# Kernel tuning notes

Hardware: AMD Instinct MI355X
Metric: run time of the kernel (lower is better)

The kernel has to match this reference:

```python
import jax, jax.numpy as jnp
import numpy as np

B, S, D = 4, 1024, 1024
H = 16
DK = D // H  # per-head dim_q = dim_k = 64
DFF = 4096
EPS = 1e-5


def _layer_norm(x, g, b):
    m = jnp.mean(x, axis=-1, keepdims=True)
    v = jnp.mean((x - m) ** 2, axis=-1, keepdims=True)
    return (x - m) / jnp.sqrt(v + EPS) * g + b


def setup_inputs() -> dict:
    key = jax.random.key(0)
    ks = jax.random.split(key, 16)
    sd = 1.0 / np.sqrt(D)
    sk = 1.0 / np.sqrt(H * DK)
    sf = 1.0 / np.sqrt(DFF)
    return {
        "src": jax.random.normal(ks[0], (B, S, D), jnp.float32),
        # stacked per-head projections (torch loops over H separate nn.Linear)
        "Wq": jax.random.uniform(ks[1], (H, D, DK), jnp.float32, -sd, sd),
        "bq": jax.random.uniform(ks[2], (H, DK), jnp.float32, -sd, sd),
        "Wk": jax.random.uniform(ks[3], (H, D, DK), jnp.float32, -sd, sd),
        "bk": jax.random.uniform(ks[4], (H, DK), jnp.float32, -sd, sd),
        "Wv": jax.random.uniform(ks[5], (H, D, DK), jnp.float32, -sd, sd),
        "bv": jax.random.uniform(ks[6], (H, DK), jnp.float32, -sd, sd),
        "Wo": jax.random.uniform(ks[7], (H * DK, D), jnp.float32, -sk, sk),
        "bo": jax.random.uniform(ks[8], (D,), jnp.float32, -sk, sk),
        "g1": jnp.ones((D,), jnp.float32),
        "be1": jnp.zeros((D,), jnp.float32),
        "W1": jax.random.uniform(ks[9], (D, DFF), jnp.float32, -sd, sd),
        "b1": jax.random.uniform(ks[10], (DFF,), jnp.float32, -sd, sd),
        "W2": jax.random.uniform(ks[11], (DFF, D), jnp.float32, -sf, sf),
        "b2": jax.random.uniform(ks[12], (D,), jnp.float32, -sf, sf),
        "g2": jnp.ones((D,), jnp.float32),
        "be2": jnp.zeros((D,), jnp.float32),
    }


def reference(src, Wq, bq, Wk, bk, Wv, bv, Wo, bo, g1, be1, W1, b1, W2, b2, g2, be2):
    # multi-head attention (all heads batched via einsum instead of python loop)
    q = jnp.einsum("bsd,hdk->bhsk", src, Wq) + bq[None, :, None, :]
    k = jnp.einsum("bsd,hdk->bhsk", src, Wk) + bk[None, :, None, :]
    v = jnp.einsum("bsd,hdk->bhsk", src, Wv) + bv[None, :, None, :]
    scale = jnp.asarray(DK, src.dtype) ** 0.5  # query.size(-1) ** 0.5
    scores = jnp.einsum("bhsk,bhtk->bhst", q, k) / scale
    attn = jax.nn.softmax(scores, axis=-1)
    o = jnp.einsum("bhst,bhtk->bhsk", attn, v)  # [B,H,S,DK]
    o = o.transpose(0, 2, 1, 3).reshape(src.shape[0], src.shape[1], H * DK)
    attn_out = o @ Wo + bo
    x = _layer_norm(src + attn_out, g1, be1)
    ffn = jax.nn.relu(x @ W1 + b1) @ W2 + b2
    return _layer_norm(x + ffn, g2, be2)
```

## Files before the change

kernel.cpp:

```cpp
#include <hip/hip_runtime.h>
#include <hip/hip_bf16.h>

#define DEV __device__ __forceinline__

typedef __attribute__((ext_vector_type(8))) short bf16x8;
typedef __attribute__((ext_vector_type(4))) float f32x4;
typedef __attribute__((ext_vector_type(4))) short short4v;
typedef __attribute__((ext_vector_type(2))) unsigned uint2v;

DEV short f2bf(float f) {
    union { float f; unsigned u; } x; x.f = f;
    unsigned u = x.u;
    unsigned r = (u + 0x7fffu + ((u >> 16) & 1u)) >> 16;
    return (short)r;
}

DEV float bf2f(short s) {
    union { unsigned u; float f; } x;
    x.u = ((unsigned)(unsigned short)s) << 16;
    return x.f;
}

DEV unsigned cvtpk(float a, float b) {
    unsigned r;
    asm("v_cvt_pk_bf16_f32 %0, %1, %2" : "=v"(r) : "v"(a), "v"(b));
    return r;
}

#define GLD16(g, l)                                                         \
    __builtin_amdgcn_global_load_lds(                                       \
        (const __attribute__((address_space(1))) void*)(g),                 \
        (__attribute__((address_space(3))) void*)(l), 16, 0, 0)

#define WAITV(n) asm volatile("s_waitcnt vmcnt(" #n ")" ::: "memory")
#define SBAR()   asm volatile("s_barrier" ::: "memory")
#define LGKMDRAIN() asm volatile("s_waitcnt lgkmcnt(0)" ::: "memory")


__global__ __launch_bounds__(256) void k_cast(const float* __restrict__ in,
                                              short* __restrict__ out, int n4) {
    int i = blockIdx.x * 256 + threadIdx.x;
    if (i >= n4) return;
    float4 v = ((const float4*)in)[i];
    short4v o;
    o[0] = f2bf(v.x); o[1] = f2bf(v.y); o[2] = f2bf(v.z); o[3] = f2bf(v.w);
    ((short4v*)out)[i] = o;
}

__global__ __launch_bounds__(256) void k_tr(const float* __restrict__ in,
                                            short* __restrict__ out,
                                            int R, int C,
                                            long in_hs, long out_hs) {
    in  += (size_t)blockIdx.z * in_hs;
    out += (size_t)blockIdx.z * out_hs;
    __shared__ short tile[64][68];
    const int t = threadIdx.x;
    const int r0 = blockIdx.y * 64, c0 = blockIdx.x * 64;
    const int lr = t >> 4, lc4 = (t & 15) * 4;
#pragma unroll
    for (int it = 0; it < 4; ++it) {
        int r = lr + it * 16;
        float4 v = *(const float4*)(in + (size_t)(r0 + r) * C + c0 + lc4);
        tile[lc4 + 0][r] = f2bf(v.x);
        tile[lc4 + 1][r] = f2bf(v.y);
        tile[lc4 + 2][r] = f2bf(v.z);
        tile[lc4 + 3][r] = f2bf(v.w);
    }
    __syncthreads();
#pragma unroll
    for (int it = 0; it < 4; ++it) {
        int c = lr + it * 16;
        short4v o;
        o[0] = tile[c][lc4 + 0];
        o[1] = tile[c][lc4 + 1];
        o[2] = tile[c][lc4 + 2];
        o[3] = tile[c][lc4 + 3];
        *(short4v*)(out + (size_t)(c0 + c) * R + r0 + lc4) = o;
    }
}

__global__ __launch_bounds__(256) void k_tr3(const float* __restrict__ Wq,
                                             const float* __restrict__ Wk,
                                             const float* __restrict__ Wv,
                                             short* __restrict__ out) {
    const int z = blockIdx.z;
    const float* in = ((z < 16) ? Wq : (z < 32) ? Wk : Wv) +
                      (size_t)(z & 15) * 65536;
    short* o = out + (size_t)z * 65536;
    __shared__ short tile[64][68];
    const int t = threadIdx.x;
    const int r0 = blockIdx.y * 64;
    const int lr = t >> 4, lc4 = (t & 15) * 4;
#pragma unroll
    for (int it = 0; it < 4; ++it) {
        int r = lr + it * 16;
        float4 v = *(const float4*)(in + (size_t)(r0 + r) * 64 + lc4);
        tile[lc4 + 0][r] = f2bf(v.x);
        tile[lc4 + 1][r] = f2bf(v.y);
        tile[lc4 + 2][r] = f2bf(v.z);
        tile[lc4 + 3][r] = f2bf(v.w);
    }
    __syncthreads();
#pragma unroll
    for (int it = 0; it < 4; ++it) {
        int c = lr + it * 16;
        short4v ov;
        ov[0] = tile[c][lc4 + 0];
        ov[1] = tile[c][lc4 + 1];
        ov[2] = tile[c][lc4 + 2];
        ov[3] = tile[c][lc4 + 3];
        *(short4v*)(o + (size_t)c * 1024 + r0 + lc4) = ov;
    }
}

template <int MODE>
__global__ __launch_bounds__(512, 2) void k_gemm8(
    const short* __restrict__ A, const short* __restrict__ BT,
    int K, int NT,
    const float* __restrict__ f0, const float* __restrict__ f1,
    const float* __restrict__ f2,
    void* __restrict__ o0, void* __restrict__ o1, void* __restrict__ o2) {
    __shared__ short lds[2][2][2][128 * 64];
    const int t = threadIdx.x;
    const int w = t >> 6, l = t & 63;
    const int l16 = l & 15, lg = l >> 4;
    const int wm = w >> 2, wn = w & 3;
    const int bn = blockIdx.x, bm = blockIdx.y;
    const int koff = blockIdx.z * NT * 64;
    const short* Ab = A + (size_t)bm * 256 * K + koff;
    const short* Bb = BT + (size_t)bn * 256 * K + koff;
    const int srow = l >> 3;
    const int scol = ((l & 7) ^ srow) * 8;
    const int offk0 = ((0 + lg) ^ (l16 & 7)) * 8;
    const int offk1 = ((4 + lg) ^ (l16 & 7)) * 8;

    f32x4 acc[8][4] = {};

    auto stg = [&](int buf, int op, int h, int kt) {
#pragma unroll
        for (int i = 0; i < 2; ++i) {
            int row = h * 128 + w * 16 + i * 8 + srow;
            GLD16((op ? Bb : Ab) + (size_t)row * K + (size_t)kt * 64 + scol,
                  &lds[buf][op][h][(w * 16 + i * 8) * 64]);
        }
    };

    stg(0, 0, 0, 0); stg(0, 0, 1, 0);
    stg(0, 1, 0, 0); stg(0, 1, 1, 0);
    const int t1p = (NT > 1) ? 1 : 0;
    stg(1, 1, 0, t1p); stg(1, 1, 1, t1p);
    WAITV(4);
    SBAR();

    for (int kt = 0; kt < NT; ++kt) {
        const int cur = kt & 1, nxt = cur ^ 1;
        const int t1 = (kt + 1 < NT) ? kt + 1 : NT - 1;
        const int t2 = (kt + 2 < NT) ? kt + 2 : NT - 1;

        stg(nxt, 0, 0, t1); stg(nxt, 0, 1, t1);

        bf16x8 a0[4][2], a1[4][2], b0[2][2], b1[2][2];
#pragma unroll
        for (int m = 0; m < 4; ++m) {
            a0[m][0] = *(const bf16x8*)&lds[cur][0][wm][(m * 16 + l16) * 64 + offk0];
            a0[m][1] = *(const bf16x8*)&lds[cur][0][wm][(m * 16 + l16) * 64 + offk1];
        }
#pragma unroll
        for (int n = 0; n < 2; ++n) {
            int r = (wn & 1) * 64 + n * 16 + l16;
            b0[n][0] = *(const bf16x8*)&lds[cur][1][wn >> 1][r * 64 + offk0];
            b0[n][1] = *(const bf16x8*)&lds[cur][1][wn >> 1][r * 64 + offk1];
            int r2 = (wn & 1) * 64 + (n + 2) * 16 + l16;
            b1[n][0] = *(const bf16x8*)&lds[cur][1][wn >> 1][r2 * 64 + offk0];
            b1[n][1] = *(const bf16x8*)&lds[cur][1][wn >> 1][r2 * 64 + offk1];
        }
        __builtin_amdgcn_s_setprio(1);
#pragma unroll
        for (int m = 0; m < 4; ++m)
#pragma unroll
            for (int n = 0; n < 2; ++n) {
                acc[m][n] = __builtin_amdgcn_mfma_f32_16x16x32_bf16(a0[m][0], b0[n][0], acc[m][n], 0, 0, 0);
                acc[m][n] = __builtin_amdgcn_mfma_f32_16x16x32_bf16(a0[m][1], b0[n][1], acc[m][n], 0, 0, 0);
                acc[m][n + 2] = __builtin_amdgcn_mfma_f32_16x16x32_bf16(a0[m][0], b1[n][0], acc[m][n + 2], 0, 0, 0);
                acc[m][n + 2] = __builtin_amdgcn_mfma_f32_16x16x32_bf16(a0[m][1], b1[n][1], acc[m][n + 2], 0, 0, 0);
            }
        __builtin_amdgcn_s_setprio(0);
#pragma unroll
        for (int m = 0; m < 4; ++m) {
            a1[m][0] = *(const bf16x8*)&lds[cur][0][wm][((m + 4) * 16 + l16) * 64 + offk0];
            a1[m][1] = *(const bf16x8*)&lds[cur][0][wm][((m + 4) * 16 + l16) * 64 + offk1];
        }
        __builtin_amdgcn_s_setprio(1);
#pragma unroll
        for (int m = 0; m < 4; ++m)
#pragma unroll
            for (int n = 0; n < 2; ++n) {
                acc[m + 4][n + 2] = __builtin_amdgcn_mfma_f32_16x16x32_bf16(a1[m][0], b1[n][0], acc[m + 4][n + 2], 0, 0, 0);
                acc[m + 4][n + 2] = __builtin_amdgcn_mfma_f32_16x16x32_bf16(a1[m][1], b1[n][1], acc[m + 4][n + 2], 0, 0, 0);
                acc[m + 4][n] = __builtin_amdgcn_mfma_f32_16x16x32_bf16(a1[m][0], b0[n][0], acc[m + 4][n], 0, 0, 0);
                acc[m + 4][n] = __builtin_amdgcn_mfma_f32_16x16x32_bf16(a1[m][1], b0[n][1], acc[m + 4][n], 0, 0, 0);
            }
        __builtin_amdgcn_s_setprio(0);

        LGKMDRAIN();
        SBAR();
        stg(cur, 1, 0, t2); stg(cur, 1, 1, t2);
        WAITV(4);
        SBAR();
    }
    WAITV(0);

    const int N = gridDim.x * 256;
#pragma unroll
    for (int m = 0; m < 8; ++m) {
        int rowbase = bm * 256 + wm * 128 + m * 16 + lg * 4;
#pragma unroll
        for (int n = 0; n < 4; ++n) {
            int col = bn * 256 + wn * 64 + n * 16 + l16;
            if constexpr (MODE == 0) {
                int p = col >> 10, c1 = col & 1023;
                int hh = c1 >> 6, dk = c1 & 63;
                const float* bias = (p == 0) ? f0 : (p == 1) ? f1 : f2;
                float bvl = bias[c1];
                float qs = (p == 0) ? 0.18033688011112042f : 1.0f;
                int b = rowbase >> 10, s = rowbase & 1023;
                if (p == 2) {
                    short4v vv;
#pragma unroll
                    for (int rr = 0; rr < 4; ++rr) vv[rr] = f2bf(acc[m][n][rr] + bvl);
                    *(short4v*)((short*)o2 + (((size_t)(b * 16 + hh) * 64 + dk) << 10) + s) = vv;
                } else {
                    short* dst = (p == 0) ? (short*)o0 : (short*)o1;
#pragma unroll
                    for (int rr = 0; rr < 4; ++rr)
                        dst[(((size_t)(b * 16 + hh) << 10) + s + rr) * 64 + dk] =
                            f2bf((acc[m][n][rr] + bvl) * qs);
                }
            } else if constexpr (MODE == 2) {
                float bvl = f0[col];
#pragma unroll
                for (int rr = 0; rr < 4; ++rr) {
                    size_t idx = (size_t)(rowbase + rr) * N + col;
                    float y = acc[m][n][rr] + bvl;
                    ((short*)o0)[idx] = f2bf(y > 0.f ? y : 0.f);
                }
            } else {
                const int Mtot = gridDim.y * 256;
                short* dst = (blockIdx.z < 3)
                    ? (short*)o0 + (size_t)blockIdx.z * Mtot * N
                    : (short*)o1;
                size_t base = (size_t)rowbase * N + col;
#pragma unroll
                for (int rr = 0; rr < 4; ++rr)
                    dst[base + (size_t)rr * N] = f2bf(acc[m][n][rr]);
            }
        }
    }
}

__global__ __launch_bounds__(512, 4) void k_attn(const short* __restrict__ Q,
                                                 const short* __restrict__ Kt,
                                                 const short* __restrict__ VT,
                                                 short* __restrict__ O) {
    __shared__ short Kl[2][64 * 64];
    __shared__ short Vl[2][64 * 64];
    __shared__ short Pl[8][16 * 64];
    const int bh = blockIdx.x;
    const int qb = blockIdx.y;
    const int t = threadIdx.x;
    const int w = t >> 6, l = t & 63;
    const int l16 = l & 15, lg = l >> 4;
    const int sw = l16 & 7;
    const int pmask = (l16 & 7) << 1;
    const int srow = l >> 3;
    const int scol = ((l & 7) ^ srow) * 8;

    const short* Qb = Q + ((size_t)bh * 1024 + qb * 128 + w * 16 + l16) * 64 + lg * 8;
    bf16x8 qf0 = *(const bf16x8*)Qb;
    bf16x8 qf1 = *(const bf16x8*)(Qb + 32);

    const short* Kbase = Kt + (size_t)bh * (1024 * 64);
    const short* Vbase = VT + (size_t)bh * (64 * 1024);

    const float THR = 11.5415603f;

    bf16x8 ones;
#pragma unroll
    for (int i = 0; i < 8; ++i) ones[i] = (short)0x3F80;

    float m = -1e30f;
    f32x4 oacc[4] = {};
    f32x4 oaccS = {};

    auto stage = [&](int buf, int t0) {
        int roww = w * 8;
        GLD16(Kbase + (size_t)(t0 + roww + srow) * 64 + scol,
              &Kl[buf][roww * 64]);
        GLD16(Vbase + (size_t)(roww + srow) * 1024 + t0 + scol,
              &Vl[buf][roww * 64]);
    };

    auto compute = [&](int cur) {
        f32x4 s[4];
#pragma unroll
        for (int n = 0; n < 4; ++n) {
            bf16x8 kf0 = *(const bf16x8*)&Kl[cur][(n * 16 + l16) * 64 + (lg ^ sw) * 8];
            bf16x8 kf1 = *(const bf16x8*)&Kl[cur][(n * 16 + l16) * 64 + ((4 + lg) ^ sw) * 8];
            f32x4 a = {0.f, 0.f, 0.f, 0.f};
            a = __builtin_amdgcn_mfma_f32_16x16x32_bf16(kf0, qf0, a, 0, 0, 0);
            a = __builtin_amdgcn_mfma_f32_16x16x32_bf16(kf1, qf1, a, 0, 0, 0);
            s[n] = a;
        }
        float m1 = fmaxf(fmaxf(s[0][0], s[0][1]), s[0][2]);
        float m2 = fmaxf(fmaxf(s[0][3], s[1][0]), s[1][1]);
        float m3 = fmaxf(fmaxf(s[1][2], s[1][3]), s[2][0]);
        float m4 = fmaxf(fmaxf(s[2][1], s[2][2]), s[2][3]);
        float m5 = fmaxf(fmaxf(s[3][0], s[3][1]), s[3][2]);
        float mx = fmaxf(fmaxf(m1, m2), m3);
        mx = fmaxf(fmaxf(m4, m5), fmaxf(mx, s[3][3]));
        mx = fmaxf(mx, __shfl_xor(mx, 16));
        mx = fmaxf(mx, __shfl_xor(mx, 32));

        if (__any(mx > m + THR)) {
            float mn = fmaxf(m, mx);
            float al = exp2f(m - mn);
            m = mn;
#pragma unroll
            for (int n = 0; n < 4; ++n)
#pragma unroll
                for (int r = 0; r < 4; ++r) s[n][r] = exp2f(s[n][r] - m);
#pragma unroll
            for (int r = 0; r < 4; ++r) {
                float alr = __shfl(al, lg * 4 + r);
                oaccS[r] *= alr;
#pragma unroll
                for (int n = 0; n < 4; ++n) oacc[n][r] *= alr;
            }
        } else {
#pragma unroll
            for (int n = 0; n < 4; ++n)
#pragma unroll
                for (int r = 0; r < 4; ++r) s[n][r] = exp2f(s[n][r] - m);
        }
#pragma unroll
        for (int n = 0; n < 4; ++n) {
            uint2v pv;
            pv[0] = cvtpk(s[n][0], s[n][1]);
            pv[1] = cvtpk(s[n][2], s[n][3]);
            int g = (n * 4 + lg) ^ pmask;
            *(uint2v*)((char*)Pl[w] + l16 * 128 + g * 8) = pv;
        }
#pragma unroll
        for (int kk = 0; kk < 2; ++kk) {
            int gp = (8 * kk + 2 * lg) ^ pmask;
            bf16x8 pa = *(const bf16x8*)((const char*)Pl[w] + l16 * 128 + gp * 8);
            oaccS = __builtin_amdgcn_mfma_f32_16x16x32_bf16(pa, ones, oaccS, 0, 0, 0);
#pragma unroll
            for (int n = 0; n < 4; ++n) {
                bf16x8 vb = *(const bf16x8*)&Vl[cur][(n * 16 + l16) * 64 +
                                                     ((kk * 4 + lg) ^ sw) * 8];
                oacc[n] = __builtin_amdgcn_mfma_f32_16x16x32_bf16(pa, vb, oacc[n],
                                                                  0, 0, 0);
            }
        }
    };

    stage(0, 0);
    for (int ti = 0; ti < 15; ++ti) {
        int cur = ti & 1;
        stage(cur ^ 1, (ti + 1) * 64);
        WAITV(2);
        SBAR();
        compute(cur);
        SBAR();
    }
    WAITV(0);
    SBAR();
    compute(1);

    const int b = bh >> 4, h = bh & 15;
#pragma unroll
    for (int r = 0; r < 4; ++r) {
        float inv = 1.f / oaccS[r];
        size_t row = (size_t)(b * 1024 + qb * 128 + w * 16 + lg * 4 + r);
#pragma unroll
        for (int n = 0; n < 4; ++n)
            O[row * 1024 + h * 64 + n * 16 + l16] = f2bf(oacc[n][r] * inv);
    }
}

__global__ __launch_bounds__(256) void k_lnwo(const short* __restrict__ p012,
                                              const short* __restrict__ p3,
                                              const float* __restrict__ bias,
                                              const float* __restrict__ resid,
                                              const float* __restrict__ g,
                                              const float* __restrict__ be,
                                              float* __restrict__ of,
                                              short* __restrict__ ob) {
    const int row = blockIdx.x, t = threadIdx.x;
    float4 x = ((const float4*)(resid + ((size_t)row << 10)))[t];
    float4 bv = ((const float4*)bias)[t];
    x.x += bv.x; x.y += bv.y; x.z += bv.z; x.w += bv.w;
#pragma unroll
    for (int kz = 0; kz < 3; ++kz) {
        short4v p = ((const short4v*)(p012 + (((size_t)kz * 4096 + row) << 10)))[t];
        x.x += bf2f(p[0]); x.y += bf2f(p[1]); x.z += bf2f(p[2]); x.w += bf2f(p[3]);
    }
    {
        short4v p = ((const short4v*)(p3 + ((size_t)row << 10)))[t];
        x.x += bf2f(p[0]); x.y += bf2f(p[1]); x.z += bf2f(p[2]); x.w += bf2f(p[3]);
    }
    float s = x.x + x.y + x.z + x.w;
    float s2 = x.x * x.x + x.y * x.y + x.z * x.z + x.w * x.w;
#pragma unroll
    for (int mm = 1; mm < 64; mm <<= 1) {
        s += __shfl_xor(s, mm);
        s2 += __shfl_xor(s2, mm);
    }
    __shared__ float red[8];
    if ((t & 63) == 0) { red[t >> 6] = s; red[4 + (t >> 6)] = s2; }
    __syncthreads();
    s = red[0] + red[1] + red[2] + red[3];
    s2 = red[4] + red[5] + red[6] + red[7];
    float mean = s * (1.f / 1024.f);
    float var = s2 * (1.f / 1024.f) - mean * mean;
    float rstd = rsqrtf(var + 1e-5f);
    int c = t * 4;
    float4 y;
    y.x = (x.x - mean) * rstd * g[c + 0] + be[c + 0];
    y.y = (x.y - mean) * rstd * g[c + 1] + be[c + 1];
    y.z = (x.z - mean) * rstd * g[c + 2] + be[c + 2];
    y.w = (x.w - mean) * rstd * g[c + 3] + be[c + 3];
    ((float4*)(of + ((size_t)row << 10)))[t] = y;
    short4v o;
    o[0] = f2bf(y.x); o[1] = f2bf(y.y); o[2] = f2bf(y.z); o[3] = f2bf(y.w);
    ((short4v*)(ob + ((size_t)row << 10)))[t] = o;
}

__global__ __launch_bounds__(256) void k_lnred(const short* __restrict__ part,
                                               const float* __restrict__ bias,
                                               const float* __restrict__ resid,
                                               const float* __restrict__ g,
                                               const float* __restrict__ be,
                                               float* __restrict__ of) {
    const int row = blockIdx.x, t = threadIdx.x;
    float4 x = ((const float4*)(resid + ((size_t)row << 10)))[t];
    float4 bv = ((const float4*)bias)[t];
    x.x += bv.x; x.y += bv.y; x.z += bv.z; x.w += bv.w;
#pragma unroll
    for (int kz = 0; kz < 4; ++kz) {
        short4v p = ((const short4v*)(part + (((size_t)kz * 4096 + row) << 10)))[t];
        x.x += bf2f(p[0]); x.y += bf2f(p[1]); x.z += bf2f(p[2]); x.w += bf2f(p[3]);
    }
    float s = x.x + x.y + x.z + x.w;
    float s2 = x.x * x.x + x.y * x.y + x.z * x.z + x.w * x.w;
#pragma unroll
    for (int mm = 1; mm < 64; mm <<= 1) {
        s += __shfl_xor(s, mm);
        s2 += __shfl_xor(s2, mm);
    }
    __shared__ float red[8];
    if ((t & 63) == 0) { red[t >> 6] = s; red[4 + (t >> 6)] = s2; }
    __syncthreads();
    s = red[0] + red[1] + red[2] + red[3];
    s2 = red[4] + red[5] + red[6] + red[7];
    float mean = s * (1.f / 1024.f);
    float var = s2 * (1.f / 1024.f) - mean * mean;
    float rstd = rsqrtf(var + 1e-5f);
    int c = t * 4;
    float4 y;
    y.x = (x.x - mean) * rstd * g[c + 0] + be[c + 0];
    y.y = (x.y - mean) * rstd * g[c + 1] + be[c + 1];
    y.z = (x.z - mean) * rstd * g[c + 2] + be[c + 2];
    y.w = (x.w - mean) * rstd * g[c + 3] + be[c + 3];
    ((float4*)(of + ((size_t)row << 10)))[t] = y;
}

extern "C" void kernel_launch(void* const* d_in, const int* in_sizes, int n_in,
                              void* d_out, int out_size, void* d_ws, size_t ws_size,
                              hipStream_t stream) {
    (void)in_sizes; (void)n_in; (void)out_size; (void)ws_size;
    const float* src = (const float*)d_in[0];
    const float* Wq  = (const float*)d_in[1];
    const float* bq  = (const float*)d_in[2];
    const float* Wk  = (const float*)d_in[3];
    const float* bk  = (const float*)d_in[4];
    const float* Wv  = (const float*)d_in[5];
    const float* bv  = (const float*)d_in[6];
    const float* Wo  = (const float*)d_in[7];
    const float* bo  = (const float*)d_in[8];
    const float* g1  = (const float*)d_in[9];
    const float* be1 = (const float*)d_in[10];
    const float* W1  = (const float*)d_in[11];
    const float* b1  = (const float*)d_in[12];
    const float* W2  = (const float*)d_in[13];
    const float* b2  = (const float*)d_in[14];
    const float* g2  = (const float*)d_in[15];
    const float* be2 = (const float*)d_in[16];

    char* ws = (char*)d_ws;
    const size_t MB = 1048576;
    short* srcbf  = (short*)(ws + 0);
    short* Qb     = (short*)(ws + 8 * MB);
    short* Kb     = (short*)(ws + 16 * MB);
    short* VTb    = (short*)(ws + 24 * MB);
    short* h1     = (short*)(ws + 0);
    short* Obuf   = srcbf;
    short* W2T    = (short*)(ws + 32 * MB);
    float* xf     = (float*)(ws + 40 * MB);
    short* WqkvT  = (short*)(ws + 56 * MB);
    short* WoT    = (short*)(ws + 62 * MB);
    short* W1T    = (short*)(ws + 64 * MB);
    short* partWo0 = (short*)(ws + 8 * MB);
    short* partWo3 = (short*)(ws + 72 * MB);
    short* xbf    = (short*)(ws + 88 * MB);
    short* part   = (short*)(ws + 56 * MB);

    k_cast<<<4096, 256, 0, stream>>>(src, srcbf, 1048576);
    k_tr3<<<dim3(1, 16, 48), 256, 0, stream>>>(Wq, Wk, Wv, WqkvT);
    k_tr<<<dim3(16, 16, 1), 256, 0, stream>>>(Wo, WoT, 1024, 1024, 0, 0);
    k_tr<<<dim3(64, 16, 1), 256, 0, stream>>>(W1, W1T, 1024, 4096, 0, 0);
    k_tr<<<dim3(16, 64, 1), 256, 0, stream>>>(W2, W2T, 4096, 1024, 0, 0);
    k_gemm8<0><<<dim3(12, 16, 1), 512, 0, stream>>>(srcbf, WqkvT, 1024, 16,
                                                    bq, bk, bv, Qb, Kb, VTb);
    k_attn<<<dim3(64, 8), 512, 0, stream>>>(Qb, Kb, VTb, Obuf);
    k_gemm8<3><<<dim3(4, 16, 4), 512, 0, stream>>>(Obuf, WoT, 1024, 4,
                                                   nullptr, nullptr, nullptr,
                                                   partWo0, partWo3, nullptr);
    k_lnwo<<<4096, 256, 0, stream>>>(partWo0, partWo3, bo, src, g1, be1, xf, xbf);
    k_gemm8<2><<<dim3(16, 16, 1), 512, 0, stream>>>(xbf, W1T, 1024, 16,
                                                    b1, nullptr, nullptr,
                                                    h1, nullptr, nullptr);
    k_gemm8<3><<<dim3(4, 16, 4), 512, 0, stream>>>(h1, W2T, 4096, 16,
                                                   nullptr, nullptr, nullptr,
                                                   part, part + 3u * 4194304u,
                                                   nullptr);
    k_lnred<<<4096, 256, 0, stream>>>(part, b2, xf, g2, be2, (float*)d_out);
}
```

Measured before the change: 209.9 us.

## Process two 16-row query tiles per wave in attention to reuse K/V fragments

Each wave in the attention kernel now handles 32 query rows as two 16-row halves. K and V fragments are loaded from LDS once and reused for both halves, which halves the LDS reads and the global K/V staging per query row. The grid shrinks to 256 blocks and launch bounds relax to 2 blocks per SM so the extra accumulator registers fit. The cost is fewer blocks and waves in flight, which reduces parallelism and latency hiding.

```diff
diff --git a/kernel.cpp b/kernel.cpp
--- a/kernel.cpp
+++ b/kernel.cpp
@@ -258,7 +258,7 @@
     }
 }
 
-__global__ __launch_bounds__(512, 4) void k_attn(const short* __restrict__ Q,
+__global__ __launch_bounds__(512, 2) void k_attn(const short* __restrict__ Q,
                                                  const short* __restrict__ Kt,
                                                  const short* __restrict__ VT,
                                                  short* __restrict__ O) {
@@ -275,9 +275,12 @@
     const int srow = l >> 3;
     const int scol = ((l & 7) ^ srow) * 8;
 
-    const short* Qb = Q + ((size_t)bh * 1024 + qb * 128 + w * 16 + l16) * 64 + lg * 8;
-    bf16x8 qf0 = *(const bf16x8*)Qb;
-    bf16x8 qf1 = *(const bf16x8*)(Qb + 32);
+    const short* Qb0 = Q + ((size_t)bh * 1024 + qb * 256 + w * 32 + l16) * 64 + lg * 8;
+    bf16x8 qf[2][2];
+    qf[0][0] = *(const bf16x8*)Qb0;
+    qf[0][1] = *(const bf16x8*)(Qb0 + 32);
+    qf[1][0] = *(const bf16x8*)(Qb0 + 16 * 64);
+    qf[1][1] = *(const bf16x8*)(Qb0 + 16 * 64 + 32);
 
     const short* Kbase = Kt + (size_t)bh * (1024 * 64);
     const short* Vbase = VT + (size_t)bh * (64 * 1024);
@@ -288,9 +291,9 @@
 #pragma unroll
     for (int i = 0; i < 8; ++i) ones[i] = (short)0x3F80;
 
-    float m = -1e30f;
-    f32x4 oacc[4] = {};
-    f32x4 oaccS = {};
+    float m[2] = {-1e30f, -1e30f};
+    f32x4 oacc[2][4] = {};
+    f32x4 oaccS[2] = {};
 
     auto stage = [&](int buf, int t0) {
         int roww = w * 8;
@@ -300,17 +303,7 @@
               &Vl[buf][roww * 64]);
     };
 
-    auto compute = [&](int cur) {
-        f32x4 s[4];
-#pragma unroll
-        for (int n = 0; n < 4; ++n) {
-            bf16x8 kf0 = *(const bf16x8*)&Kl[cur][(n * 16 + l16) * 64 + (lg ^ sw) * 8];
-            bf16x8 kf1 = *(const bf16x8*)&Kl[cur][(n * 16 + l16) * 64 + ((4 + lg) ^ sw) * 8];
-            f32x4 a = {0.f, 0.f, 0.f, 0.f};
-            a = __builtin_amdgcn_mfma_f32_16x16x32_bf16(kf0, qf0, a, 0, 0, 0);
-            a = __builtin_amdgcn_mfma_f32_16x16x32_bf16(kf1, qf1, a, 0, 0, 0);
-            s[n] = a;
-        }
+    auto softmax = [&](f32x4 (&s)[4], int h) {
         float m1 = fmaxf(fmaxf(s[0][0], s[0][1]), s[0][2]);
         float m2 = fmaxf(fmaxf(s[0][3], s[1][0]), s[1][1]);
         float m3 = fmaxf(fmaxf(s[1][2], s[1][3]), s[2][0]);
@@ -320,28 +313,30 @@
         mx = fmaxf(fmaxf(m4, m5), fmaxf(mx, s[3][3]));
         mx = fmaxf(mx, __shfl_xor(mx, 16));
         mx = fmaxf(mx, __shfl_xor(mx, 32));
-
-        if (__any(mx > m + THR)) {
-            float mn = fmaxf(m, mx);
-            float al = exp2f(m - mn);
-            m = mn;
+        if (__any(mx > m[h] + THR)) {
+            float mn = fmaxf(m[h], mx);
+            float al = exp2f(m[h] - mn);
+            m[h] = mn;
 #pragma unroll
             for (int n = 0; n < 4; ++n)
 #pragma unroll
-                for (int r = 0; r < 4; ++r) s[n][r] = exp2f(s[n][r] - m);
+                for (int r = 0; r < 4; ++r) s[n][r] = exp2f(s[n][r] - mn);
 #pragma unroll
             for (int r = 0; r < 4; ++r) {
                 float alr = __shfl(al, lg * 4 + r);
-                oaccS[r] *= alr;
-#pragma unroll
-                for (int n = 0; n < 4; ++n) oacc[n][r] *= alr;
+                oaccS[h][r] *= alr;
+#pragma unroll
+                for (int n = 0; n < 4; ++n) oacc[h][n][r] *= alr;
             }
         } else {
 #pragma unroll
             for (int n = 0; n < 4; ++n)
 #pragma unroll
-                for (int r = 0; r < 4; ++r) s[n][r] = exp2f(s[n][r] - m);
-        }
+                for (int r = 0; r < 4; ++r) s[n][r] = exp2f(s[n][r] - m[h]);
+        }
+    };
+
+    auto pwrite = [&](const f32x4 (&s)[4]) {
 #pragma unroll
         for (int n = 0; n < 4; ++n) {
             uint2v pv;
@@ -350,18 +345,58 @@
             int g = (n * 4 + lg) ^ pmask;
             *(uint2v*)((char*)Pl[w] + l16 * 128 + g * 8) = pv;
         }
+    };
+
+    auto compute = [&](int cur) {
+        bf16x8 kf[4][2];
+#pragma unroll
+        for (int n = 0; n < 4; ++n) {
+            kf[n][0] = *(const bf16x8*)&Kl[cur][(n * 16 + l16) * 64 + (lg ^ sw) * 8];
+            kf[n][1] = *(const bf16x8*)&Kl[cur][(n * 16 + l16) * 64 + ((4 + lg) ^ sw) * 8];
+        }
+        f32x4 s0[4], s1[4];
+#pragma unroll
+        for (int n = 0; n < 4; ++n) {
+            f32x4 a = {0.f, 0.f, 0.f, 0.f};
+            a = __builtin_amdgcn_mfma_f32_16x16x32_bf16(kf[n][0], qf[0][0], a, 0, 0, 0);
+            a = __builtin_amdgcn_mfma_f32_16x16x32_bf16(kf[n][1], qf[0][1], a, 0, 0, 0);
+            s0[n] = a;
+        }
+#pragma unroll
+        for (int n = 0; n < 4; ++n) {
+            f32x4 a = {0.f, 0.f, 0.f, 0.f};
+            a = __builtin_amdgcn_mfma_f32_16x16x32_bf16(kf[n][0], qf[1][0], a, 0, 0, 0);
+            a = __builtin_amdgcn_mfma_f32_16x16x32_bf16(kf[n][1], qf[1][1], a, 0, 0, 0);
+            s1[n] = a;
+        }
+        softmax(s0, 0);
+        softmax(s1, 1);
+        bf16x8 vb[2][4];
+#pragma unroll
+        for (int kk = 0; kk < 2; ++kk)
+#pragma unroll
+            for (int n = 0; n < 4; ++n)
+                vb[kk][n] = *(const bf16x8*)&Vl[cur][(n * 16 + l16) * 64 +
+                                                     ((kk * 4 + lg) ^ sw) * 8];
+        pwrite(s0);
 #pragma unroll
         for (int kk = 0; kk < 2; ++kk) {
             int gp = (8 * kk + 2 * lg) ^ pmask;
             bf16x8 pa = *(const bf16x8*)((const char*)Pl[w] + l16 * 128 + gp * 8);
-            oaccS = __builtin_amdgcn_mfma_f32_16x16x32_bf16(pa, ones, oaccS, 0, 0, 0);
-#pragma unroll
-            for (int n = 0; n < 4; ++n) {
-                bf16x8 vb = *(const bf16x8*)&Vl[cur][(n * 16 + l16) * 64 +
-                                                     ((kk * 4 + lg) ^ sw) * 8];
-                oacc[n] = __builtin_amdgcn_mfma_f32_16x16x32_bf16(pa, vb, oacc[n],
-                                                                  0, 0, 0);
-            }
+            oaccS[0] = __builtin_amdgcn_mfma_f32_16x16x32_bf16(pa, ones, oaccS[0], 0, 0, 0);
+#pragma unroll
+            for (int n = 0; n < 4; ++n)
+                oacc[0][n] = __builtin_amdgcn_mfma_f32_16x16x32_bf16(pa, vb[kk][n], oacc[0][n], 0, 0, 0);
+        }
+        pwrite(s1);
+#pragma unroll
+        for (int kk = 0; kk < 2; ++kk) {
+            int gp = (8 * kk + 2 * lg) ^ pmask;
+            bf16x8 pa = *(const bf16x8*)((const char*)Pl[w] + l16 * 128 + gp * 8);
+            oaccS[1] = __builtin_amdgcn_mfma_f32_16x16x32_bf16(pa, ones, oaccS[1], 0, 0, 0);
+#pragma unroll
+            for (int n = 0; n < 4; ++n)
+                oacc[1][n] = __builtin_amdgcn_mfma_f32_16x16x32_bf16(pa, vb[kk][n], oacc[1][n], 0, 0, 0);
         }
     };
 
@@ -380,13 +415,16 @@
 
     const int b = bh >> 4, h = bh & 15;
 #pragma unroll
-    for (int r = 0; r < 4; ++r) {
-        float inv = 1.f / oaccS[r];
-        size_t row = (size_t)(b * 1024 + qb * 128 + w * 16 + lg * 4 + r);
-#pragma unroll
-        for (int n = 0; n < 4; ++n)
-            O[row * 1024 + h * 64 + n * 16 + l16] = f2bf(oacc[n][r] * inv);
-    }
+    for (int qh = 0; qh < 2; ++qh)
+#pragma unroll
+        for (int r = 0; r < 4; ++r) {
+            float inv = 1.f / oaccS[qh][r];
+            size_t row = (size_t)(b * 1024 + qb * 256 + w * 32 + qh * 16 +
+                                  lg * 4 + r);
+#pragma unroll
+            for (int n = 0; n < 4; ++n)
+                O[row * 1024 + h * 64 + n * 16 + l16] = f2bf(oacc[qh][n][r] * inv);
+        }
 }
 
 __global__ __launch_bounds__(256) void k_lnwo(const short* __restrict__ p012,
@@ -523,7 +561,7 @@
     k_tr<<<dim3(16, 64, 1), 256, 0, stream>>>(W2, W2T, 4096, 1024, 0, 0);
     k_gemm8<0><<<dim3(12, 16, 1), 512, 0, stream>>>(srcbf, WqkvT, 1024, 16,
                                                     bq, bk, bv, Qb, Kb, VTb);
-    k_attn<<<dim3(64, 8), 512, 0, stream>>>(Qb, Kb, VTb, Obuf);
+    k_attn<<<dim3(64, 4), 512, 0, stream>>>(Qb, Kb, VTb, Obuf);
     k_gemm8<3><<<dim3(4, 16, 4), 512, 0, stream>>>(Obuf, WoT, 1024, 4,
                                                    nullptr, nullptr, nullptr,
                                                    partWo0, partWo3, nullptr);
```

Result: slower. 362.6 us (+72.7%).
